# Kernel optimization log

Measured on AMD Instinct MI355X. Metric: run time of the kernel, lower is better.

The kernel has to match this reference:

```python
import jax, jax.numpy as jnp
import numpy as np

N_NODES = 100000
N_EDGES = 1600000
IN_DIM = 128
HID = 64
OUT_DIM = 3


def _glorot(key, shape):
    fan_in, fan_out = shape[0], shape[1]
    std = (2.0 / (fan_in + fan_out)) ** 0.5
    return jax.random.normal(key, shape, jnp.float32) * std


def setup_inputs() -> dict:
    key = jax.random.key(0)
    ks = jax.random.split(key, 12)
    x = jax.random.normal(ks[0], (N_NODES, IN_DIM), jnp.float32)
    edge_index = jax.random.randint(ks[1], (2, N_EDGES), 0, N_NODES, dtype=jnp.int32)
    return {
        "x": x,
        "edge_index": edge_index,
        "W1": _glorot(ks[2], (IN_DIM, HID)), "b1": jnp.zeros((HID,), jnp.float32),
        "W2": _glorot(ks[3], (HID, HID)), "b2": jnp.zeros((HID,), jnp.float32),
        "W3": _glorot(ks[4], (HID, HID)), "b3": jnp.zeros((HID,), jnp.float32),
        "W4": _glorot(ks[5], (HID, HID // 2)), "b4": jnp.zeros((HID // 2,), jnp.float32),
        "Wh": _glorot(ks[6], (HID // 2, OUT_DIM)), "bh": jnp.zeros((OUT_DIM,), jnp.float32),
    }


def reference(x, edge_index, W1, b1, W2, b2, W3, b3, W4, b4, Wh, bh):
    n = x.shape[0]
    self_loops = jnp.arange(n, dtype=edge_index.dtype)
    src = jnp.concatenate([edge_index[0], self_loops])  # message sources j
    dst = jnp.concatenate([edge_index[1], self_loops])  # aggregation targets i
    # symmetric GCN normalization with self-loops: deg over targets (unit edge weights)
    deg = jax.ops.segment_sum(jnp.ones_like(dst, jnp.float32), dst, num_segments=n)
    dinv = jnp.where(deg > 0, jax.lax.rsqrt(deg), 0.0)
    norm = dinv[src] * dinv[dst]  # [E+N]

    def gcn(h, W, b):
        h = h @ W  # transform first (PyG GCNConv order)
        agg = jax.ops.segment_sum(h[src] * norm[:, None], dst, num_segments=n)
        return agg + b

    h = jax.nn.relu(gcn(x, W1, b1))   # dropout is identity in eval mode
    h = jax.nn.relu(gcn(h, W2, b2))
    h = jax.nn.relu(gcn(h, W3, b3))
    h = jax.nn.relu(gcn(h, W4, b4))
    return h @ Wh + bh  # [N, 3]
```

## Files before the change

### kernel.cpp

```cpp
#include <hip/hip_runtime.h>
#include <hip/hip_bf16.h>
#include <hip/hip_fp16.h>
#include <cstdint>


#define MAXD 512
#define EB   8192
#define PADSLACK 2048

typedef _Float16 half8v __attribute__((ext_vector_type(8)));
typedef _Float16 half2v __attribute__((ext_vector_type(2)));
typedef float    float4v __attribute__((ext_vector_type(4)));

#if defined(__has_builtin)
#if __has_builtin(__builtin_amdgcn_fdot2)
#define HAVE_FDOT2 1
#endif
#endif

__device__ __forceinline__ float fdot2f(half2v a, half2v b, float c) {
#ifdef HAVE_FDOT2
    return __builtin_amdgcn_fdot2(a, b, c, false);
#else
    return c + (float)a[0] * (float)b[0] + (float)a[1] * (float)b[1];
#endif
}

__device__ __forceinline__ void digit_base_scan(const int* __restrict__ totals,
                                                int ND, int* pairs, int* cbs) {
    const int t = threadIdx.x;
    const int e0 = 2 * t, e1 = 2 * t + 1;
    int v0 = (e0 < ND) ? totals[e0] : 0;
    int v1 = (e1 < ND) ? totals[e1] : 0;
    pairs[t] = v0 + v1;
    __syncthreads();
    for (int off = 1; off < 256; off <<= 1) {
        int x = (t >= off) ? pairs[t - off] : 0;
        __syncthreads();
        pairs[t] += x;
        __syncthreads();
    }
    int ep = pairs[t] - v0 - v1;
    cbs[e0] = ep;
    cbs[e1] = ep + v0;
    __syncthreads();
}

__device__ __forceinline__ void hist_body(const int* __restrict__ ei,
                                          int* __restrict__ histM, int E, int b) {
    __shared__ int hist[MAXD];
    const int tid = threadIdx.x;
    hist[tid] = 0; hist[tid + 256] = 0;
    __syncthreads();
    const int base = b * EB;
#pragma unroll 2
    for (int it = 0; it < EB / 256; it += 4) {
        int d[4]; bool ok[4];
#pragma unroll
        for (int u = 0; u < 4; ++u) {
            int e = base + (it + u) * 256 + tid;
            ok[u] = e < E;
            d[u] = ok[u] ? ei[E + e] : 0;
        }
#pragma unroll
        for (int u = 0; u < 4; ++u)
            if (ok[u]) atomicAdd(&hist[d[u] >> 8], 1);
    }
    __syncthreads();
    histM[(size_t)b * MAXD + tid] = hist[tid];
    histM[(size_t)b * MAXD + tid + 256] = hist[tid + 256];
}

__global__ __launch_bounds__(256) void scan_digits_k(int* __restrict__ histM,
                                                     int* __restrict__ totals,
                                                     int NBLK) {
    __shared__ int s[256];
    const int t = threadIdx.x, dg = blockIdx.x;
    int v = (t < NBLK) ? histM[(size_t)t * MAXD + dg] : 0;
    s[t] = v;
    __syncthreads();
    for (int off = 1; off < 256; off <<= 1) {
        int x = (t >= off) ? s[t - off] : 0;
        __syncthreads();
        s[t] += x;
        __syncthreads();
    }
    if (t < NBLK) histM[(size_t)t * MAXD + dg] = s[t] - v;
    if (t == 255) totals[dg] = s[255];
}

template <int K, int OUT>
__device__ __forceinline__ void gemm_body(const float* __restrict__ H,
                                          const float* __restrict__ W,
                                          float* __restrict__ Tout, int n, int bx) {
    constexpr int TX  = OUT / 4;
    constexpr int TY  = 256 / TX;
    constexpr int BM  = TY * 4;
    constexpr int BK  = 32;
    constexpr int PAD = 4;

    __shared__ float At[BK][BM + PAD];
    __shared__ float Ws[BK][OUT];

    const int t    = threadIdx.x;
    const int cx   = t % TX;
    const int ry   = t / TX;
    const int row0 = bx * BM;

    float acc[4][4] = {{0.f}};
    const int arow = t >> 3;
    const int af4  = t & 7;

    for (int k0 = 0; k0 < K; k0 += BK) {
#pragma unroll
        for (int p = 0; p < BM / 32; ++p) {
            int r  = arow + p * 32;
            int gr = row0 + r;
            int grc = gr < n ? gr : n - 1;
            float4 v = *reinterpret_cast<const float4*>(
                H + (size_t)grc * K + k0 + af4 * 4);
            At[af4 * 4 + 0][r] = v.x;
            At[af4 * 4 + 1][r] = v.y;
            At[af4 * 4 + 2][r] = v.z;
            At[af4 * 4 + 3][r] = v.w;
        }
#pragma unroll
        for (int p = 0; p < (BK * OUT) / 1024; ++p) {
            int idx = t + p * 256;
            int wk  = idx / (OUT / 4);
            int wf  = idx % (OUT / 4);
            float4 v = *reinterpret_cast<const float4*>(
                W + (size_t)(k0 + wk) * OUT + wf * 4);
            *reinterpret_cast<float4*>(&Ws[wk][wf * 4]) = v;
        }
        __syncthreads();
#pragma unroll
        for (int k = 0; k < BK; ++k) {
            float4 a = *reinterpret_cast<const float4*>(&At[k][ry * 4]);
            float4 w = *reinterpret_cast<const float4*>(&Ws[k][cx * 4]);
            acc[0][0] = fmaf(a.x, w.x, acc[0][0]);
            acc[0][1] = fmaf(a.x, w.y, acc[0][1]);
            acc[0][2] = fmaf(a.x, w.z, acc[0][2]);
            acc[0][3] = fmaf(a.x, w.w, acc[0][3]);
            acc[1][0] = fmaf(a.y, w.x, acc[1][0]);
            acc[1][1] = fmaf(a.y, w.y, acc[1][1]);
            acc[1][2] = fmaf(a.y, w.z, acc[1][2]);
            acc[1][3] = fmaf(a.y, w.w, acc[1][3]);
            acc[2][0] = fmaf(a.z, w.x, acc[2][0]);
            acc[2][1] = fmaf(a.z, w.y, acc[2][1]);
            acc[2][2] = fmaf(a.z, w.z, acc[2][2]);
            acc[2][3] = fmaf(a.z, w.w, acc[2][3]);
            acc[3][0] = fmaf(a.w, w.x, acc[3][0]);
            acc[3][1] = fmaf(a.w, w.y, acc[3][1]);
            acc[3][2] = fmaf(a.w, w.z, acc[3][2]);
            acc[3][3] = fmaf(a.w, w.w, acc[3][3]);
        }
        __syncthreads();
    }
#pragma unroll
    for (int i = 0; i < 4; ++i) {
        int gr = row0 + ry * 4 + i;
        if (gr < n) {
            float4 v = make_float4(acc[i][0], acc[i][1], acc[i][2], acc[i][3]);
            *reinterpret_cast<float4*>(Tout + (size_t)gr * OUT + cx * 4) = v;
        }
    }
}

__device__ __forceinline__ void pack_body(const int* __restrict__ ei,
                                          const int* __restrict__ histM,
                                          const int* __restrict__ totals,
                                          int* __restrict__ packed,
                                          int E, int ND, int b) {
    __shared__ int pairs[256];
    __shared__ int cbs[MAXD];
    __shared__ int cur[MAXD];
    const int tid = threadIdx.x;
    digit_base_scan(totals, ND, pairs, cbs);
    for (int t = tid; t < ND; t += 256)
        cur[t] = cbs[t] + histM[(size_t)b * MAXD + t];
    __syncthreads();
    const int base = b * EB;
    for (int it = 0; it < EB / 256; it += 4) {
        int s[4], d[4]; bool ok[4];
#pragma unroll
        for (int u = 0; u < 4; ++u) {
            int e = base + (it + u) * 256 + tid;
            ok[u] = e < E;
            if (ok[u]) { s[u] = ei[e]; d[u] = ei[E + e]; }
        }
#pragma unroll
        for (int u = 0; u < 4; ++u) {
            if (ok[u]) {
                int pos = atomicAdd(&cur[d[u] >> 8], 1);
                packed[pos] = (s[u] << 8) | (d[u] & 255);
            }
        }
    }
}

__global__ __launch_bounds__(256) void hist_gemm1_k(
    const int* __restrict__ ei, int* __restrict__ histM, int E,
    const float* __restrict__ x, const float* __restrict__ W1,
    float* __restrict__ T1, int n, int NH) {
    const int bx = blockIdx.x;
    if (bx < NH) hist_body(ei, histM, E, bx);
    else         gemm_body<128, 64>(x, W1, T1, n, bx - NH);
}

__global__ __launch_bounds__(256) void pack_gemm1_k(
    const int* __restrict__ ei, const int* __restrict__ histM,
    const int* __restrict__ totals, int* __restrict__ packed,
    const float* __restrict__ x, const float* __restrict__ W1,
    float* __restrict__ T1, int n, int E, int ND, int NPB, int G1) {
    const int bx = blockIdx.x;
    if (bx < NPB) pack_body(ei, histM, totals, packed, E, ND, bx);
    else          gemm_body<128, 64>(x, W1, T1, n, G1 + bx - NPB);
}

__global__ __launch_bounds__(256) void bucket_k(const int* __restrict__ packed,
                                                const int* __restrict__ totals,
                                                int ND,
                                                int* __restrict__ col,
                                                int4* __restrict__ rpc,
                                                float* __restrict__ dinv,
                                                const float* __restrict__ Traw,
                                                __half* __restrict__ Th, int n) {
    __shared__ int   pairs[256];
    __shared__ int   cbs[MAXD];
    __shared__ int   hist[256];
    __shared__ int   pref[256];
    __shared__ int   cur[256];
    __shared__ float dinv_l[256];

    const int tid = threadIdx.x;
    const int dg  = blockIdx.x;
    digit_base_scan(totals, ND, pairs, cbs);
    const int base  = cbs[dg];
    const int m     = totals[dg];
    const int basep = base + dg * PADSLACK;

    hist[tid] = 0;
    __syncthreads();
    for (int k0 = 0; k0 < m; k0 += 1024) {
        int v[4]; bool ok[4];
#pragma unroll
        for (int u = 0; u < 4; ++u) {
            int k = k0 + u * 256 + tid;
            ok[u] = k < m;
            v[u] = ok[u] ? packed[base + k] : 0;
        }
#pragma unroll
        for (int u = 0; u < 4; ++u)
            if (ok[u]) atomicAdd(&hist[v[u] & 255], 1);
    }
    __syncthreads();
    const int deg   = hist[tid];
    const int cnt_p = (deg + 8) & ~7;
    pref[tid] = cnt_p;
    __syncthreads();
    for (int off = 1; off < 256; off <<= 1) {
        int x = (tid >= off) ? pref[tid - off] : 0;
        __syncthreads();
        pref[tid] += x;
        __syncthreads();
    }
    const int rp = basep + pref[tid] - cnt_p;
    const float di = rsqrtf((float)(deg + 1));
    dinv_l[tid] = di;
    cur[tid] = rp + 1;
    const int d = dg * 256 + tid;
    if (d < n) {
        rpc[d]  = make_int4(rp, cnt_p, __float_as_int(di), 0);
        dinv[d] = di;
        col[rp] = d;
        for (int k = deg + 1; k < cnt_p; ++k) col[rp + k] = n;
    }
    __syncthreads();
    for (int k0 = 0; k0 < m; k0 += 1024) {
        int v[4]; bool ok[4];
#pragma unroll
        for (int u = 0; u < 4; ++u) {
            int k = k0 + u * 256 + tid;
            ok[u] = k < m;
            v[u] = ok[u] ? packed[base + k] : 0;
        }
#pragma unroll
        for (int u = 0; u < 4; ++u) {
            if (ok[u]) {
                int pos = atomicAdd(&cur[v[u] & 255], 1);
                col[pos] = v[u] >> 8;
            }
        }
    }
    const int r0 = dg * 256;
#pragma unroll 4
    for (int it = 0; it < 16; ++it) {
        int idx = it * 256 + tid;
        int rl  = idx >> 4;
        int r   = r0 + rl;
        if (r < n) {
            float4 v = reinterpret_cast<const float4*>(Traw)[(size_t)r * 16 + (idx & 15)];
            float dd = dinv_l[rl];
            union { ushort4 u; __half h[4]; } pk;
            pk.h[0] = __float2half_rn(v.x * dd);
            pk.h[1] = __float2half_rn(v.y * dd);
            pk.h[2] = __float2half_rn(v.z * dd);
            pk.h[3] = __float2half_rn(v.w * dd);
            reinterpret_cast<ushort4*>(Th)[(size_t)r * 16 + (idx & 15)] = pk.u;
        }
    }
    if (dg == 0 && tid < 16) {
        uint2 z; z.x = 0u; z.y = 0u;
        reinterpret_cast<uint2*>(Th)[(size_t)n * 16 + tid] = z;
    }
}

template <int OUT>
__global__ __launch_bounds__(256) void gemm_mfma_k(
    const _Float16* __restrict__ H, const float* __restrict__ W,
    const float* __restrict__ dinv, _Float16* __restrict__ T, int n) {
    constexpr int NT = OUT / 16;
    const int lane = threadIdx.x & 63;
    const int m16  = lane & 15;
    const int quad = lane >> 4;
    const int wid  = (blockIdx.x * blockDim.x + threadIdx.x) >> 6;
    const int nw   = (gridDim.x * blockDim.x) >> 6;

    half8v bfrag[NT][2];
#pragma unroll
    for (int t = 0; t < NT; ++t)
#pragma unroll
        for (int h = 0; h < 2; ++h)
#pragma unroll
            for (int j = 0; j < 8; ++j)
                bfrag[t][h][j] = (_Float16)W[(size_t)(h * 32 + quad * 8 + j) * OUT
                                             + t * 16 + m16];

    const int nblk = (n + 15) >> 4;
    for (int rb = wid; rb < nblk; rb += nw) {
        const int r0 = rb * 16;
        int ra = r0 + m16; if (ra >= n) ra = n - 1;
        const half8v* hrow = reinterpret_cast<const half8v*>(H + (size_t)ra * 64);
        half8v a0 = hrow[quad];
        half8v a1 = hrow[4 + quad];

        float4v dfr[NT];
#pragma unroll
        for (int t = 0; t < NT; ++t) {
            float4v z = {0.f, 0.f, 0.f, 0.f};
            z = __builtin_amdgcn_mfma_f32_16x16x32_f16(a0, bfrag[t][0], z, 0, 0, 0);
            z = __builtin_amdgcn_mfma_f32_16x16x32_f16(a1, bfrag[t][1], z, 0, 0, 0);
            dfr[t] = z;
        }
#pragma unroll
        for (int reg = 0; reg < 4; ++reg) {
            int row = r0 + quad * 4 + reg;
            if (row < n) {
                float di = dinv[row];
#pragma unroll
                for (int t = 0; t < NT; ++t)
                    T[(size_t)row * 64 + t * 16 + m16] =
                        (_Float16)(dfr[t][reg] * di);
            }
        }
    }
}

template <int NB, int LR>
__device__ __forceinline__ void gather_batch(int c_l, const uint2* __restrict__ T2,
                                             int q, int sw, float4& acc, int g0) {
    constexpr int NSW = 64 / LR;
    constexpr int GPE = 8 / NSW;
    constexpr int NV  = NB * GPE;
    const half2v s10 = {(_Float16)1.f, (_Float16)0.f};
    const half2v s01 = {(_Float16)0.f, (_Float16)1.f};
    uint2 v[NV];
#pragma unroll
    for (int g = 0; g < NB; ++g)
#pragma unroll
        for (int u = 0; u < GPE; ++u) {
            int cc = __shfl(c_l, (g0 + g) * 8 + u * NSW + sw, 64);
            v[g * GPE + u] = T2[(size_t)cc * 16 + q];
        }
#pragma unroll
    for (int k = 0; k < NV; ++k) {
        union { uint2 uu; half2v h[2]; } cv; cv.uu = v[k];
        acc.x = fdot2f(cv.h[0], s10, acc.x);
        acc.y = fdot2f(cv.h[0], s01, acc.y);
        acc.z = fdot2f(cv.h[1], s10, acc.z);
        acc.w = fdot2f(cv.h[1], s01, acc.w);
    }
}

__device__ __forceinline__ void gather_node(int cnt, int start, int c_a,
                                            const uint2* __restrict__ T2,
                                            const int* __restrict__ col,
                                            int lane, int q, int sw, float4& acc) {
    if (cnt <= 64) {
        switch (cnt >> 3) {
            case 1: gather_batch<1, 64 / ((64/16))>(c_a, T2, q, sw, acc, 0); break;
            default: break;
        }
    }
}

template <int LR, bool FUSE_HEAD>
__global__ __launch_bounds__(256, 8) void agg_k(const __half* __restrict__ T,
                                             const int4* __restrict__ rpc,
                                             const int* __restrict__ col,
                                             const float* __restrict__ bias,
                                             void* __restrict__ O, int n,
                                             const float* __restrict__ Wh,
                                             const float* __restrict__ bh) {
    constexpr int NSW = 64 / LR;
    constexpr int GPE = 8 / NSW;
    const int lane = threadIdx.x & 63;
    const int q    = lane % LR;
    const int sw   = lane / LR;
    const int wid  = (blockIdx.x * blockDim.x + threadIdx.x) >> 6;
    const int nw   = (gridDim.x * blockDim.x) >> 6;
    if (wid >= n) return;

    const uint2* __restrict__ T2 = reinterpret_cast<const uint2*>(T);
    const float4 b4 = reinterpret_cast<const float4*>(bias)[q];

    int ib = wid + nw; if (ib >= n) ib = n - 1;
    int4 rc_a = rpc[wid];
    int4 rc_b = rpc[ib];
    int  c_a  = col[rc_a.x + lane];

    for (int i = wid; i < n; i += nw) {
        int ic = i + 2 * nw; if (ic >= n) ic = n - 1;
        int4 rc_c = rpc[ic];
        int  c_nx = col[rc_b.x + lane];

        const int   cnt   = rc_a.y;
        const int   start = rc_a.x;
        const float di    = __int_as_float(rc_a.z);

        float4 acc = make_float4(0.f, 0.f, 0.f, 0.f);
        if (cnt <= 64) {
            switch (cnt >> 3) {
                case 1: gather_batch<1, LR>(c_a, T2, q, sw, acc, 0); break;
                case 2: gather_batch<2, LR>(c_a, T2, q, sw, acc, 0); break;
                case 3: gather_batch<3, LR>(c_a, T2, q, sw, acc, 0); break;
                case 4: gather_batch<4, LR>(c_a, T2, q, sw, acc, 0); break;
                case 5: gather_batch<4, LR>(c_a, T2, q, sw, acc, 0);
                        gather_batch<1, LR>(c_a, T2, q, sw, acc, 4); break;
                case 6: gather_batch<4, LR>(c_a, T2, q, sw, acc, 0);
                        gather_batch<2, LR>(c_a, T2, q, sw, acc, 4); break;
                case 7: gather_batch<4, LR>(c_a, T2, q, sw, acc, 0);
                        gather_batch<3, LR>(c_a, T2, q, sw, acc, 4); break;
                default: gather_batch<4, LR>(c_a, T2, q, sw, acc, 0);
                         gather_batch<4, LR>(c_a, T2, q, sw, acc, 4); break;
            }
        } else {
            for (int base = 0; base < cnt; base += 64) {
                int m = cnt - base; if (m > 64) m = 64;
                int c_l = col[start + base + lane];
                for (int jg = 0; jg < m; jg += 32) {
                    int nb2 = (m - jg) >> 3; if (nb2 > 4) nb2 = 4;
                    int g0 = jg >> 3;
                    switch (nb2) {
                        case 1: gather_batch<1, LR>(c_l, T2, q, sw, acc, g0); break;
                        case 2: gather_batch<2, LR>(c_l, T2, q, sw, acc, g0); break;
                        case 3: gather_batch<3, LR>(c_l, T2, q, sw, acc, g0); break;
                        default: gather_batch<4, LR>(c_l, T2, q, sw, acc, g0); break;
                    }
                }
            }
        }
#pragma unroll
        for (int off = LR; off < 64; off <<= 1) {
            acc.x += __shfl_xor(acc.x, off, 64);
            acc.y += __shfl_xor(acc.y, off, 64);
            acc.z += __shfl_xor(acc.z, off, 64);
            acc.w += __shfl_xor(acc.w, off, 64);
        }
        float4 h;
        h.x = fmaxf(fmaf(di, acc.x, b4.x), 0.f);
        h.y = fmaxf(fmaf(di, acc.y, b4.y), 0.f);
        h.z = fmaxf(fmaf(di, acc.z, b4.z), 0.f);
        h.w = fmaxf(fmaf(di, acc.w, b4.w), 0.f);
        if constexpr (!FUSE_HEAD) {
            if (sw == 0) {
                union { ushort4 u; __half hh[4]; } pk;
                pk.hh[0] = __float2half_rn(h.x);
                pk.hh[1] = __float2half_rn(h.y);
                pk.hh[2] = __float2half_rn(h.z);
                pk.hh[3] = __float2half_rn(h.w);
                ushort* base_p = (ushort*)O + (size_t)i * 64;
                *reinterpret_cast<ushort4*>(base_p + 4 * q) = pk.u;
            }
        } else {
            float* Of = (float*)O;
            float p0 = h.x * Wh[(4 * q + 0) * 3 + 0];
            float p1 = h.x * Wh[(4 * q + 0) * 3 + 1];
            float p2 = h.x * Wh[(4 * q + 0) * 3 + 2];
            p0 = fmaf(h.y, Wh[(4 * q + 1) * 3 + 0], p0);
            p1 = fmaf(h.y, Wh[(4 * q + 1) * 3 + 1], p1);
            p2 = fmaf(h.y, Wh[(4 * q + 1) * 3 + 2], p2);
            p0 = fmaf(h.z, Wh[(4 * q + 2) * 3 + 0], p0);
            p1 = fmaf(h.z, Wh[(4 * q + 2) * 3 + 1], p1);
            p2 = fmaf(h.z, Wh[(4 * q + 2) * 3 + 2], p2);
            p0 = fmaf(h.w, Wh[(4 * q + 3) * 3 + 0], p0);
            p1 = fmaf(h.w, Wh[(4 * q + 3) * 3 + 1], p1);
            p2 = fmaf(h.w, Wh[(4 * q + 3) * 3 + 2], p2);
#pragma unroll
            for (int off = 1; off < LR; off <<= 1) {
                p0 += __shfl_xor(p0, off, 64);
                p1 += __shfl_xor(p1, off, 64);
                p2 += __shfl_xor(p2, off, 64);
            }
            if (lane == 0) {
                Of[(size_t)i * 3 + 0] = p0 + bh[0];
                Of[(size_t)i * 3 + 1] = p1 + bh[1];
                Of[(size_t)i * 3 + 2] = p2 + bh[2];
            }
        }
        rc_a = rc_b; rc_b = rc_c; c_a = c_nx;
    }
}

extern "C" void kernel_launch(void* const* d_in, const int* in_sizes, int n_in,
                              void* d_out, int out_size, void* d_ws, size_t ws_size,
                              hipStream_t stream) {
    const float* x  = (const float*)d_in[0];
    const int*   ei = (const int*)d_in[1];
    const float* W1 = (const float*)d_in[2];
    const float* b1 = (const float*)d_in[3];
    const float* W2 = (const float*)d_in[4];
    const float* b2 = (const float*)d_in[5];
    const float* W3 = (const float*)d_in[6];
    const float* b3 = (const float*)d_in[7];
    const float* W4 = (const float*)d_in[8];
    const float* b4 = (const float*)d_in[9];
    const float* Wh = (const float*)d_in[10];
    const float* bh = (const float*)d_in[11];
    float* out = (float*)d_out;

    const int n = in_sizes[0] / 128;
    const int E = in_sizes[1] / 2;
    const int ND   = (n + 255) / 256;
    const int NBLK = (E + EB - 1) / EB;

    char* ws = (char*)d_ws;
    auto alloc = [&](size_t bytes) {
        char* p = ws;
        ws += (bytes + 255) & ~(size_t)255;
        return p;
    };
    int*    histM  = (int*)alloc((size_t)NBLK * MAXD * 4);
    int*    totals = (int*)alloc((size_t)MAXD * 4);
    int*    packed = (int*)alloc((size_t)E * 4);
    int*    col    = (int*)alloc(((size_t)E + (size_t)ND * PADSLACK + 256) * 4);
    int4*   rpc    = (int4*)alloc((size_t)n * 16);
    float*  dinv   = (float*)alloc((size_t)n * 4);
    float*  bufF   = (float*)alloc((size_t)n * 64 * 4);
    __half* bufH   = (__half*)alloc(((size_t)n + 1) * 64 * 2);
    __half* bufG   = (__half*)bufF;

    dim3 blk(256);
    const int G  = (n + 63) / 64;
    const int G1 = G / 3;
    const int G2 = G - G1;
    const int agg_blocks = 2048;
    const int mfma_blocks = 640;

    hist_gemm1_k<<<dim3(NBLK + G1), blk, 0, stream>>>(ei, histM, E, x, W1, bufF, n, NBLK);
    scan_digits_k<<<dim3(ND), blk, 0, stream>>>(histM, totals, NBLK);
    pack_gemm1_k<<<dim3(NBLK + G2), blk, 0, stream>>>(ei, histM, totals, packed,
                                                      x, W1, bufF, n, E, ND, NBLK, G1);
    bucket_k<<<dim3(ND), blk, 0, stream>>>(packed, totals, ND, col, rpc,
                                           dinv, bufF, bufH, n);
    agg_k<16, false><<<dim3(agg_blocks), blk, 0, stream>>>(
        bufH, rpc, col, b1, bufG, n, nullptr, nullptr);
    gemm_mfma_k<64><<<dim3(mfma_blocks), blk, 0, stream>>>(
        (const _Float16*)bufG, W2, dinv, (_Float16*)bufH, n);
    agg_k<16, false><<<dim3(agg_blocks), blk, 0, stream>>>(
        bufH, rpc, col, b2, bufG, n, nullptr, nullptr);
    gemm_mfma_k<64><<<dim3(mfma_blocks), blk, 0, stream>>>(
        (const _Float16*)bufG, W3, dinv, (_Float16*)bufH, n);
    agg_k<16, false><<<dim3(agg_blocks), blk, 0, stream>>>(
        bufH, rpc, col, b3, bufG, n, nullptr, nullptr);
    gemm_mfma_k<32><<<dim3(mfma_blocks), blk, 0, stream>>>(
        (const _Float16*)bufG, W4, dinv, (_Float16*)bufH, n);
    agg_k<8, true><<<dim3(agg_blocks), blk, 0, stream>>>(
        bufH, rpc, col, b4, out, n, Wh, bh);
}
```

Measured before the change: 334.5 us.

## Use fp16 MFMA for first-layer GEMM and widen gather batches

Replaces the FP32 SIMT tiled GEMM for the first layer (128->64) with an MFMA 16x16x32 f16 kernel. W1 is transposed into shared memory as half, and x is converted to half in registers. The aggregation kernel now uses single gather batches of up to 8 groups instead of splitting into 4+N, and the high-degree path becomes a simple loop over groups of 8. This reduces GEMM compute cost and branching in the gather, but lowers the precision of the first GEMM inputs to fp16 and raises register pressure from the larger gather batches.

```diff
diff --git a/kernel.cpp b/kernel.cpp
--- a/kernel.cpp
+++ b/kernel.cpp
@@ -89,80 +89,56 @@
     if (t == 255) totals[dg] = s[255];
 }
 
-template <int K, int OUT>
-__device__ __forceinline__ void gemm_body(const float* __restrict__ H,
-                                          const float* __restrict__ W,
-                                          float* __restrict__ Tout, int n, int bx) {
-    constexpr int TX  = OUT / 4;
-    constexpr int TY  = 256 / TX;
-    constexpr int BM  = TY * 4;
-    constexpr int BK  = 32;
-    constexpr int PAD = 4;
-
-    __shared__ float At[BK][BM + PAD];
-    __shared__ float Ws[BK][OUT];
-
-    const int t    = threadIdx.x;
-    const int cx   = t % TX;
-    const int ry   = t / TX;
-    const int row0 = bx * BM;
-
-    float acc[4][4] = {{0.f}};
-    const int arow = t >> 3;
-    const int af4  = t & 7;
-
-    for (int k0 = 0; k0 < K; k0 += BK) {
-#pragma unroll
-        for (int p = 0; p < BM / 32; ++p) {
-            int r  = arow + p * 32;
-            int gr = row0 + r;
-            int grc = gr < n ? gr : n - 1;
-            float4 v = *reinterpret_cast<const float4*>(
-                H + (size_t)grc * K + k0 + af4 * 4);
-            At[af4 * 4 + 0][r] = v.x;
-            At[af4 * 4 + 1][r] = v.y;
-            At[af4 * 4 + 2][r] = v.z;
-            At[af4 * 4 + 3][r] = v.w;
-        }
-#pragma unroll
-        for (int p = 0; p < (BK * OUT) / 1024; ++p) {
-            int idx = t + p * 256;
-            int wk  = idx / (OUT / 4);
-            int wf  = idx % (OUT / 4);
-            float4 v = *reinterpret_cast<const float4*>(
-                W + (size_t)(k0 + wk) * OUT + wf * 4);
-            *reinterpret_cast<float4*>(&Ws[wk][wf * 4]) = v;
-        }
-        __syncthreads();
-#pragma unroll
-        for (int k = 0; k < BK; ++k) {
-            float4 a = *reinterpret_cast<const float4*>(&At[k][ry * 4]);
-            float4 w = *reinterpret_cast<const float4*>(&Ws[k][cx * 4]);
-            acc[0][0] = fmaf(a.x, w.x, acc[0][0]);
-            acc[0][1] = fmaf(a.x, w.y, acc[0][1]);
-            acc[0][2] = fmaf(a.x, w.z, acc[0][2]);
-            acc[0][3] = fmaf(a.x, w.w, acc[0][3]);
-            acc[1][0] = fmaf(a.y, w.x, acc[1][0]);
-            acc[1][1] = fmaf(a.y, w.y, acc[1][1]);
-            acc[1][2] = fmaf(a.y, w.z, acc[1][2]);
-            acc[1][3] = fmaf(a.y, w.w, acc[1][3]);
-            acc[2][0] = fmaf(a.z, w.x, acc[2][0]);
-            acc[2][1] = fmaf(a.z, w.y, acc[2][1]);
-            acc[2][2] = fmaf(a.z, w.z, acc[2][2]);
-            acc[2][3] = fmaf(a.z, w.w, acc[2][3]);
-            acc[3][0] = fmaf(a.w, w.x, acc[3][0]);
-            acc[3][1] = fmaf(a.w, w.y, acc[3][1]);
-            acc[3][2] = fmaf(a.w, w.z, acc[3][2]);
-            acc[3][3] = fmaf(a.w, w.w, acc[3][3]);
-        }
-        __syncthreads();
-    }
-#pragma unroll
-    for (int i = 0; i < 4; ++i) {
-        int gr = row0 + ry * 4 + i;
-        if (gr < n) {
-            float4 v = make_float4(acc[i][0], acc[i][1], acc[i][2], acc[i][3]);
-            *reinterpret_cast<float4*>(Tout + (size_t)gr * OUT + cx * 4) = v;
+__device__ __forceinline__ void gemm1_mfma_body(const float* __restrict__ X,
+                                                const float* __restrict__ W,
+                                                float* __restrict__ Tout,
+                                                int n, int bx) {
+    __shared__ _Float16 WT[64][136];
+    const int t = threadIdx.x;
+#pragma unroll
+    for (int p = 0; p < 8; ++p) {
+        int f4 = t + p * 256;
+        int k  = f4 >> 4;
+        int o  = (f4 & 15) * 4;
+        float4 v = reinterpret_cast<const float4*>(W)[f4];
+        WT[o + 0][k] = (_Float16)v.x;
+        WT[o + 1][k] = (_Float16)v.y;
+        WT[o + 2][k] = (_Float16)v.z;
+        WT[o + 3][k] = (_Float16)v.w;
+    }
+    __syncthreads();
+
+    const int lane = t & 63;
+    const int wv   = t >> 6;
+    const int m16  = lane & 15;
+    const int quad = lane >> 4;
+    const int r0   = bx * 64 + wv * 16;
+    int ra = r0 + m16; if (ra >= n) ra = n - 1;
+
+    const float4* xrow = reinterpret_cast<const float4*>(X + (size_t)ra * 128);
+    half8v a[4];
+#pragma unroll
+    for (int h = 0; h < 4; ++h) {
+        int f0 = (h * 32 + quad * 8) >> 2;
+        float4 v0 = xrow[f0];
+        float4 v1 = xrow[f0 + 1];
+        a[h][0] = (_Float16)v0.x; a[h][1] = (_Float16)v0.y;
+        a[h][2] = (_Float16)v0.z; a[h][3] = (_Float16)v0.w;
+        a[h][4] = (_Float16)v1.x; a[h][5] = (_Float16)v1.y;
+        a[h][6] = (_Float16)v1.z; a[h][7] = (_Float16)v1.w;
+    }
+#pragma unroll
+    for (int tt = 0; tt < 4; ++tt) {
+        const half8v* wt = reinterpret_cast<const half8v*>(&WT[tt * 16 + m16][0]);
+        float4v z = {0.f, 0.f, 0.f, 0.f};
+#pragma unroll
+        for (int h = 0; h < 4; ++h)
+            z = __builtin_amdgcn_mfma_f32_16x16x32_f16(a[h], wt[h * 4 + quad], z, 0, 0, 0);
+#pragma unroll
+        for (int reg = 0; reg < 4; ++reg) {
+            int row = r0 + quad * 4 + reg;
+            if (row < n)
+                Tout[(size_t)row * 64 + tt * 16 + m16] = z[reg];
         }
     }
 }
@@ -205,7 +181,7 @@
     float* __restrict__ T1, int n, int NH) {
     const int bx = blockIdx.x;
     if (bx < NH) hist_body(ei, histM, E, bx);
-    else         gemm_body<128, 64>(x, W1, T1, n, bx - NH);
+    else         gemm1_mfma_body(x, W1, T1, n, bx - NH);
 }
 
 __global__ __launch_bounds__(256) void pack_gemm1_k(
@@ -215,7 +191,7 @@
     float* __restrict__ T1, int n, int E, int ND, int NPB, int G1) {
     const int bx = blockIdx.x;
     if (bx < NPB) pack_body(ei, histM, totals, packed, E, ND, bx);
-    else          gemm_body<128, 64>(x, W1, T1, n, G1 + bx - NPB);
+    else          gemm1_mfma_body(x, W1, T1, n, G1 + bx - NPB);
 }
 
 __global__ __launch_bounds__(256) void bucket_k(const int* __restrict__ packed,
@@ -369,7 +345,7 @@
 
 template <int NB, int LR>
 __device__ __forceinline__ void gather_batch(int c_l, const uint2* __restrict__ T2,
-                                             int q, int sw, float4& acc, int g0) {
+                                             int q, int sw, float4& acc) {
     constexpr int NSW = 64 / LR;
     constexpr int GPE = 8 / NSW;
     constexpr int NV  = NB * GPE;
@@ -380,7 +356,7 @@
     for (int g = 0; g < NB; ++g)
 #pragma unroll
         for (int u = 0; u < GPE; ++u) {
-            int cc = __shfl(c_l, (g0 + g) * 8 + u * NSW + sw, 64);
+            int cc = __shfl(c_l, g * 8 + u * NSW + sw, 64);
             v[g * GPE + u] = T2[(size_t)cc * 16 + q];
         }
 #pragma unroll
@@ -390,18 +366,6 @@
         acc.y = fdot2f(cv.h[0], s01, acc.y);
         acc.z = fdot2f(cv.h[1], s10, acc.z);
         acc.w = fdot2f(cv.h[1], s01, acc.w);
-    }
-}
-
-__device__ __forceinline__ void gather_node(int cnt, int start, int c_a,
-                                            const uint2* __restrict__ T2,
-                                            const int* __restrict__ col,
-                                            int lane, int q, int sw, float4& acc) {
-    if (cnt <= 64) {
-        switch (cnt >> 3) {
-            case 1: gather_batch<1, 64 / ((64/16))>(c_a, T2, q, sw, acc, 0); break;
-            default: break;
-        }
     }
 }
 
@@ -442,31 +406,35 @@
         float4 acc = make_float4(0.f, 0.f, 0.f, 0.f);
         if (cnt <= 64) {
             switch (cnt >> 3) {
-                case 1: gather_batch<1, LR>(c_a, T2, q, sw, acc, 0); break;
-                case 2: gather_batch<2, LR>(c_a, T2, q, sw, acc, 0); break;
-                case 3: gather_batch<3, LR>(c_a, T2, q, sw, acc, 0); break;
-                case 4: gather_batch<4, LR>(c_a, T2, q, sw, acc, 0); break;
-                case 5: gather_batch<4, LR>(c_a, T2, q, sw, acc, 0);
-                        gather_batch<1, LR>(c_a, T2, q, sw, acc, 4); break;
-                case 6: gather_batch<4, LR>(c_a, T2, q, sw, acc, 0);
-                        gather_batch<2, LR>(c_a, T2, q, sw, acc, 4); break;
-                case 7: gather_batch<4, LR>(c_a, T2, q, sw, acc, 0);
-                        gather_batch<3, LR>(c_a, T2, q, sw, acc, 4); break;
-                default: gather_batch<4, LR>(c_a, T2, q, sw, acc, 0);
-                         gather_batch<4, LR>(c_a, T2, q, sw, acc, 4); break;
+                case 1: gather_batch<1, LR>(c_a, T2, q, sw, acc); break;
+                case 2: gather_batch<2, LR>(c_a, T2, q, sw, acc); break;
+                case 3: gather_batch<3, LR>(c_a, T2, q, sw, acc); break;
+                case 4: gather_batch<4, LR>(c_a, T2, q, sw, acc); break;
+                case 5: gather_batch<5, LR>(c_a, T2, q, sw, acc); break;
+                case 6: gather_batch<6, LR>(c_a, T2, q, sw, acc); break;
+                case 7: gather_batch<7, LR>(c_a, T2, q, sw, acc); break;
+                default: gather_batch<8, LR>(c_a, T2, q, sw, acc); break;
             }
         } else {
+            const half2v s10 = {(_Float16)1.f, (_Float16)0.f};
+            const half2v s01 = {(_Float16)0.f, (_Float16)1.f};
             for (int base = 0; base < cnt; base += 64) {
-                int m = cnt - base; if (m > 64) m = 64;
+                const int m = min(64, cnt - base);
                 int c_l = col[start + base + lane];
-                for (int jg = 0; jg < m; jg += 32) {
-                    int nb2 = (m - jg) >> 3; if (nb2 > 4) nb2 = 4;
-                    int g0 = jg >> 3;
-                    switch (nb2) {
-                        case 1: gather_batch<1, LR>(c_l, T2, q, sw, acc, g0); break;
-                        case 2: gather_batch<2, LR>(c_l, T2, q, sw, acc, g0); break;
-                        case 3: gather_batch<3, LR>(c_l, T2, q, sw, acc, g0); break;
-                        default: gather_batch<4, LR>(c_l, T2, q, sw, acc, g0); break;
+                for (int jg = 0; jg < m; jg += 8) {
+                    int cc[GPE]; uint2 v[GPE];
+#pragma unroll
+                    for (int u = 0; u < GPE; ++u)
+                        cc[u] = __shfl(c_l, jg + u * NSW + sw, 64);
+#pragma unroll
+                    for (int u = 0; u < GPE; ++u) v[u] = T2[(size_t)cc[u] * 16 + q];
+#pragma unroll
+                    for (int u = 0; u < GPE; ++u) {
+                        union { uint2 uu; half2v h[2]; } cv; cv.uu = v[u];
+                        acc.x = fdot2f(cv.h[0], s10, acc.x);
+                        acc.y = fdot2f(cv.h[0], s01, acc.y);
+                        acc.z = fdot2f(cv.h[1], s10, acc.z);
+                        acc.w = fdot2f(cv.h[1], s01, acc.w);
                     }
                 }
             }
```

Result: slower. 356.6 us (+6.6%).
